# Kernel tuning notes

Hardware: AMD Instinct MI355X
Metric: run time of the kernel (lower is better)

The kernel has to match this reference:

```python
import jax, jax.numpy as jnp
import numpy as np

D_MODEL = 1024
NUM_HEADS = 8
D_K = D_MODEL // NUM_HEADS
NEG_INF = -1e9
EPS = 1e-6


def setup_inputs() -> dict:
    key = jax.random.key(0)
    ks = jax.random.split(key, 10)
    B, S = 4, 2048
    scale = 1.0 / np.sqrt(D_MODEL)
    return {
        "queries": jax.random.normal(ks[0], (B, S, D_MODEL), jnp.float32),
        "keys": jax.random.normal(ks[1], (B, S, D_MODEL), jnp.float32),
        "values": jax.random.normal(ks[2], (B, S, D_MODEL), jnp.float32),
        "Wq": jax.random.normal(ks[3], (D_MODEL, D_MODEL), jnp.float32) * scale,
        "bq": jnp.zeros((D_MODEL,), jnp.float32),
        "Wk": jax.random.normal(ks[4], (D_MODEL, D_MODEL), jnp.float32) * scale,
        "bk": jnp.zeros((D_MODEL,), jnp.float32),
        "Wv": jax.random.normal(ks[5], (D_MODEL, D_MODEL), jnp.float32) * scale,
        "bv": jnp.zeros((D_MODEL,), jnp.float32),
        "gamma": jnp.ones((D_MODEL,), jnp.float32),
        "beta": jnp.zeros((D_MODEL,), jnp.float32),
    }


def _split_heads(x, B, S):
    # [B,S,D] -> [B,H,S,d_k]
    return x.reshape(B, S, NUM_HEADS, D_K).transpose(0, 2, 1, 3)


def reference(queries, keys, values, Wq, bq, Wk, bk, Wv, bv, gamma, beta):
    B, S, _ = queries.shape
    Q = _split_heads(queries @ Wq + bq, B, S)
    K = _split_heads(keys @ Wk + bk, B, keys.shape[1])
    V = _split_heads(values @ Wv + bv, B, values.shape[1])
    scores = jnp.einsum("bhqd,bhkd->bhqk", Q, K) / jnp.sqrt(jnp.float32(D_K))
    # causal mask (lower triangular kept)
    Sk = scores.shape[-1]
    mask = jnp.tril(jnp.ones((scores.shape[-2], Sk), dtype=bool))
    scores = jnp.where(mask, scores, jnp.float32(NEG_INF))
    attn = jax.nn.softmax(scores, axis=-1)
    # dropout disabled (training=False)
    out = jnp.einsum("bhqk,bhkd->bhqd", attn, V)
    out = out.transpose(0, 2, 1, 3).reshape(B, S, D_MODEL)
    resid = out + queries
    mu = jnp.mean(resid, axis=-1, keepdims=True)
    var = jnp.var(resid, axis=-1, keepdims=True)
    normed = (resid - mu) / jnp.sqrt(var + EPS)
    return normed * gamma + beta
```

## Files before the change

### kernel.cpp

```cpp
#include <hip/hip_runtime.h>
#include <hip/hip_bf16.h>
#include <stdint.h>

#define D_MODEL 1024
#define S_LEN   2048
#define BATCH   4
#define NH      8
#define DK      128

typedef __attribute__((ext_vector_type(8))) __bf16 bf16x8;
typedef __attribute__((ext_vector_type(4))) float  f32x4;

__device__ __forceinline__ f32x4 mfma16(bf16x8 a, bf16x8 b, f32x4 c) {
  return __builtin_amdgcn_mfma_f32_16x16x32_bf16(a, b, c, 0, 0, 0);
}

__device__ __forceinline__ void gld_lds16(const void* g, void* l) {
  __builtin_amdgcn_global_load_lds(
      (const __attribute__((address_space(1))) void*)g,
      (__attribute__((address_space(3))) void*)l, 16, 0, 0);
}

#define ATTN_SCALE 0.08838834764831845f

__global__ __launch_bounds__(256) void cvt_kernel(
    const float* __restrict__ x0, const float* __restrict__ x1,
    const float* __restrict__ x2, __hip_bfloat16* __restrict__ out) {
  const size_t N = (size_t)BATCH * S_LEN * D_MODEL;
  const int w = blockIdx.y;
  const float* src = (w == 0) ? x0 : (w == 1) ? x1 : x2;
  __hip_bfloat16* dst = out + (size_t)w * N;
  const size_t i = ((size_t)blockIdx.x * 256 + threadIdx.x) * 4;
  const float4 v = *(const float4*)(src + i);
  *(__hip_bfloat162*)(dst + i)     = __float22bfloat162_rn(make_float2(v.x, v.y));
  *(__hip_bfloat162*)(dst + i + 2) = __float22bfloat162_rn(make_float2(v.z, v.w));
}

__global__ void wtrans_kernel(const float* __restrict__ Wq,
                              const float* __restrict__ Wk,
                              const float* __restrict__ Wv,
                              __hip_bfloat16* __restrict__ Wt) {
  __shared__ __hip_bfloat16 tile[32][33];
  const int w = blockIdx.z;
  const float* src = (w == 0) ? Wq : (w == 1) ? Wk : Wv;
  const float sc = (w == 0) ? ATTN_SCALE : 1.0f;
  __hip_bfloat16* dst = Wt + (size_t)w * D_MODEL * D_MODEL;
  const int tx = threadIdx.x, ty = threadIdx.y;
  int x = blockIdx.x * 32 + tx;
  int y = blockIdx.y * 32 + ty;
  for (int i = 0; i < 32; i += 8)
    tile[ty + i][tx] = __float2bfloat16(src[(size_t)(y + i) * D_MODEL + x] * sc);
  __syncthreads();
  x = blockIdx.y * 32 + tx;
  y = blockIdx.x * 32 + ty;
  for (int i = 0; i < 32; i += 8)
    dst[(size_t)(y + i) * D_MODEL + x] = tile[tx][ty + i];
}

__global__ __launch_bounds__(256) void qkv_gemm_kernel(
    const __hip_bfloat16* __restrict__ Xbf,
    const float* __restrict__ bq, const float* __restrict__ bk,
    const float* __restrict__ bv,
    const __hip_bfloat16* __restrict__ Wt,
    __hip_bfloat16* __restrict__ Qo, __hip_bfloat16* __restrict__ Ko,
    __hip_bfloat16* __restrict__ Vo) {
  const int flat = blockIdx.x;
  const int xcd  = flat & 7;
  const int idx  = flat >> 3;
  const int n_t  = idx & 7;
  const int mg   = idx >> 3;
  const int pair = xcd * 24 + mg;
  const int which = pair >> 6;
  const int m_t   = pair & 63;

  const size_t N = (size_t)BATCH * S_LEN * D_MODEL;
  const __hip_bfloat16* X = Xbf + (size_t)which * N;
  const __hip_bfloat16* W = Wt + (size_t)which * D_MODEL * D_MODEL;
  const float* bias = (which == 0) ? bq : (which == 1) ? bk : bv;
  const float bscale = (which == 0) ? ATTN_SCALE : 1.0f;

  __shared__ __align__(16) char smem[128 * 136 * 2];
  __hip_bfloat16* Asm = (__hip_bfloat16*)smem;
  __hip_bfloat16* Bsm = Asm + 128 * 64;
  __hip_bfloat16* Cb  = (__hip_bfloat16*)smem;

  const int tid  = threadIdx.x;
  const int lane = tid & 63;
  const int wv   = tid >> 6;
  const int lo16 = lane & 15;
  const int hi4  = lane >> 4;
  const int m0 = m_t * 128;
  const int n0 = n_t * 128;
  const int wm = (wv >> 1) * 64;
  const int wn = (wv & 1) * 64;

  f32x4 acc[4][4];
  const f32x4 z4 = {0.f, 0.f, 0.f, 0.f};
  for (int i = 0; i < 4; ++i)
    for (int j = 0; j < 4; ++j) acc[i][j] = z4;

  for (int k0 = 0; k0 < D_MODEL; k0 += 64) {
    __syncthreads();
    for (int it = 0; it < 4; ++it) {
      const int cbase = it * 256 + wv * 64;
      const int c = cbase + lane;
      const int row = c >> 3;
      const int kc = ((c & 7) ^ (row & 7)) * 8;
      gld_lds16(X + (size_t)(m0 + row) * D_MODEL + k0 + kc, &Asm[cbase * 8]);
      gld_lds16(W + (size_t)(n0 + row) * D_MODEL + k0 + kc, &Bsm[cbase * 8]);
    }
    __syncthreads();

    for (int kk = 0; kk < 2; ++kk) {
      bf16x8 af[4], bfr[4];
      const int sl = (kk * 4 + hi4);
      for (int i = 0; i < 4; ++i) {
        const int lm = wm + 16 * i + lo16;
        af[i] = *(const bf16x8*)&Asm[lm * 64 + ((sl ^ (lm & 7)) * 8)];
      }
      for (int j = 0; j < 4; ++j) {
        const int ln = wn + 16 * j + lo16;
        bfr[j] = *(const bf16x8*)&Bsm[ln * 64 + ((sl ^ (ln & 7)) * 8)];
      }
      for (int i = 0; i < 4; ++i)
        for (int j = 0; j < 4; ++j)
          acc[i][j] = mfma16(af[i], bfr[j], acc[i][j]);
    }
  }

  const int b  = m0 >> 11;
  const int s0 = m0 & (S_LEN - 1);
  const int h  = n0 >> 7;
  const size_t bh = (size_t)(b * NH + h);

  __syncthreads();
  for (int j = 0; j < 4; ++j) {
    const int nl = wn + 16 * j + lo16;
    const float bval = bias[n0 + nl] * bscale;
    for (int i = 0; i < 4; ++i) {
      for (int r = 0; r < 4; ++r) {
        const int lm = wm + 16 * i + hi4 * 4 + r;
        const __hip_bfloat16 ob = __float2bfloat16(acc[i][j][r] + bval);
        if (which == 2) {
          const int col = (lm & 96) + 2 * (lm & 15) + ((lm >> 4) & 1);
          Cb[nl * 136 + col] = ob;
        } else {
          Cb[lm * 136 + nl] = ob;
        }
      }
    }
  }
  __syncthreads();

  if (which == 0) {
    __hip_bfloat16* gq = Qo + (bh * S_LEN + s0) * DK;
    for (int r8 = 0; r8 < 8; ++r8) {
      const int C = r8 * 256 + tid;
      const bf16x8 v = *(const bf16x8*)&Cb[(C >> 4) * 136 + (C & 15) * 8];
      *(bf16x8*)&gq[(size_t)C * 8] = v;
    }
  } else if (which == 1) {
    __hip_bfloat16* gk = Ko + (bh * 64 + (s0 >> 5)) * 4096;
    for (int r8 = 0; r8 < 8; ++r8) {
      const int C = r8 * 256 + tid;
      const int su = C >> 9, Cw = C & 511;
      const bf16x8 v =
          *(const bf16x8*)&Cb[(su * 32 + (Cw & 31)) * 136 + (Cw >> 5) * 8];
      *(bf16x8*)&gk[(size_t)su * 4096 + (Cw >> 5) * 256 + (Cw & 31) * 8] = v;
    }
  } else {
    __hip_bfloat16* gv = Vo + (bh * 64 + (s0 >> 5)) * 4096;
    for (int r8 = 0; r8 < 8; ++r8) {
      const int C = r8 * 256 + tid;
      const int su = C >> 9, Cw = C & 511;
      const bf16x8 v =
          *(const bf16x8*)&Cb[(C & 127) * 136 + su * 32 + (Cw >> 7) * 8];
      *(bf16x8*)&gv[(size_t)su * 4096 + (size_t)Cw * 8] = v;
    }
  }
}

__device__ const uint32_t ATTN_TBL[24] = {
  79, 95, 32,
  78, 94, 33,
  77, 93, 34,
  76, 92, 35,
  75, 91, 36,
  39, 72, 88,
  38, 73, 89,
  37, 74, 90
};

__global__ __launch_bounds__(256, 3) void attn_kernel(
    const __hip_bfloat16* __restrict__ Qw, const __hip_bfloat16* __restrict__ Kw,
    const __hip_bfloat16* __restrict__ Vtw, __hip_bfloat16* __restrict__ Og,
    float* __restrict__ partO, float* __restrict__ lsumP) {
  const int bid = blockIdx.x;
  const int q8  = bid & 255;
  const int rr  = bid >> 8;
  const int bh  = q8 & 31;
  const int jrow = q8 >> 5;
  const int h   = bh & 7;
  const int b   = bh >> 3;
  const uint32_t wi = ATTN_TBL[jrow * 3 + rr];
  const int  t     = wi & 15;
  const int  chnk  = (wi >> 4) & 1;
  const bool split = (wi >> 5) == 2;
  const int  half  = 2 * t + 2;
  const int  st0   = (split && chnk == 1) ? half : 0;
  const int  stN   = (split && chnk == 0) ? half : (4 * t + 4);

  const int tid  = threadIdx.x;
  const int lane = tid & 63;
  const int wv   = tid >> 6;
  const int lo16 = lane & 15;
  const int hi4  = lane >> 4;

  const int qrow0 = t * 128 + wv * 32;
  const int ns_w  = 4 * t + wv + 1;

  const size_t bhp = (size_t)(b * NH + h);
  const __hip_bfloat16* Qp = Qw + bhp * S_LEN * DK;
  const __hip_bfloat16* Kp = Kw + bhp * S_LEN * DK;
  const __hip_bfloat16* Vp = Vtw + bhp * S_LEN * DK;

  __shared__ __align__(16) __hip_bfloat16 Ksm[2][32 * 128];
  __shared__ __align__(16) __hip_bfloat16 Psm[4][32 * 40];

  bf16x8 qf[2][4];
  for (int m = 0; m < 2; ++m)
    for (int kk = 0; kk < 4; ++kk)
      qf[m][kk] = *(const bf16x8*)&Qp[(size_t)(qrow0 + m * 16 + lo16) * DK +
                                      kk * 32 + hi4 * 8];

  f32x4 oacc[2][8];
  const f32x4 z4 = {0.f, 0.f, 0.f, 0.f};
  for (int m = 0; m < 2; ++m)
    for (int j = 0; j < 8; ++j) oacc[m][j] = z4;
  float lsum[2][4];
  for (int m = 0; m < 2; ++m)
    for (int i = 0; i < 4; ++i) lsum[m][i] = 0.f;

  const __hip_bfloat16* kbase[2];
#pragma unroll
  for (int it = 0; it < 2; ++it)
    kbase[it] = Kp + (size_t)(it * 256 + tid) * 8;
  auto stage = [&](int st, int buf) {
#pragma unroll
    for (int it = 0; it < 2; ++it) {
      const int cb = (it * 256 + wv * 64) * 8;
      gld_lds16(kbase[it] + ((size_t)st << 12), &Ksm[buf][cb]);
    }
  };

  stage(st0, 0);

  int bsel = 0;
  for (int st = st0; st < stN; ++st) {
    asm volatile("s_waitcnt vmcnt(0)" ::: "memory");
    __builtin_amdgcn_s_barrier();
    asm volatile("" ::: "memory");

    const bool act = st < ns_w;

    bf16x8 vf[8];
    if (act) {
      const __hip_bfloat16* vt = Vp + ((size_t)st << 12);
#pragma unroll
      for (int j = 0; j < 8; ++j)
        vf[j] = *(const bf16x8*)&vt[(hi4 * 128 + j * 16 + lo16) * 8];
    }
    if (st + 1 < stN) stage(st + 1, bsel ^ 1);

    if (act) {
      const __hip_bfloat16* Kb = Ksm[bsel];

      bf16x8 kf[2][4];
      for (int kn = 0; kn < 2; ++kn)
        for (int kk = 0; kk < 4; ++kk)
          kf[kn][kk] = *(const bf16x8*)&Kb[((kk * 4 + hi4) * 32 + kn * 16 + lo16) * 8];
      f32x4 sc[2][2];
      for (int m = 0; m < 2; ++m)
        for (int kn = 0; kn < 2; ++kn) {
          f32x4 s4 = z4;
          for (int kk = 0; kk < 4; ++kk)
            s4 = mfma16(qf[m][kk], kf[kn][kk], s4);
          sc[m][kn] = s4;
        }

      const int kv0 = st << 5;
      const bool do_mask = (st == ns_w - 1);
      for (int m = 0; m < 2; ++m) {
        for (int i = 0; i < 4; ++i) {
          const int qg = qrow0 + m * 16 + hi4 * 4 + i;
          float s0 = sc[m][0][i];
          float s1 = sc[m][1][i];
          if (do_mask) {
            if (kv0 + lo16 > qg)      s0 = -1.0e30f;
            if (kv0 + 16 + lo16 > qg) s1 = -1.0e30f;
          }
          const float p0 = __expf(s0 - 8.f);
          const float p1 = __expf(s1 - 8.f);
          lsum[m][i] += p0 + p1;
          const int prw = m * 16 + hi4 * 4 + i;
          *(__hip_bfloat162*)&Psm[wv][prw * 40 + 2 * lo16] =
              __float22bfloat162_rn(make_float2(p0, p1));
        }
      }
      asm volatile("s_waitcnt lgkmcnt(0)" ::: "memory");

      bf16x8 pf[2];
      for (int m = 0; m < 2; ++m)
        pf[m] = *(const bf16x8*)&Psm[wv][(m * 16 + lo16) * 40 + hi4 * 8];
      for (int j = 0; j < 8; ++j) {
        oacc[0][j] = mfma16(pf[0], vf[j], oacc[0][j]);
        oacc[1][j] = mfma16(pf[1], vf[j], oacc[1][j]);
      }
    }
    bsel ^= 1;
  }

  for (int m = 0; m < 2; ++m) {
    for (int i = 0; i < 4; ++i) {
      float l = lsum[m][i];
      l += __shfl_xor(l, 1);
      l += __shfl_xor(l, 2);
      l += __shfl_xor(l, 4);
      l += __shfl_xor(l, 8);
      const int row = wv * 32 + m * 16 + hi4 * 4 + i;
      if (!split) {
        const float inv = 1.0f / l;
        const int qg = t * 128 + row;
        __hip_bfloat16* orow = Og + ((size_t)b * S_LEN + qg) * D_MODEL + h * DK;
        for (int j = 0; j < 8; ++j)
          orow[j * 16 + lo16] = __float2bfloat16(oacc[m][j][i] * inv);
      } else {
        const int pidx = bh * 8 + (t - 8);
        float* prow = partO +
            (((size_t)chnk * 256 + pidx) * 128 + row) * 128;
        for (int j = 0; j < 8; ++j)
          prow[j * 16 + lo16] = oacc[m][j][i];
        if (lo16 == 0)
          lsumP[(chnk * 256 + pidx) * 128 + row] = l;
      }
    }
  }
}

__global__ __launch_bounds__(256) void ln_kernel(
    const __hip_bfloat16* __restrict__ Og, const float* __restrict__ partO,
    const float* __restrict__ lsumP, const float* __restrict__ resid_in,
    const float* __restrict__ gamma, const float* __restrict__ beta,
    float* __restrict__ out) {
  const int row  = blockIdx.x;
  const int b    = row >> 11;
  const int srow = row & (S_LEN - 1);
  const int tile = srow >> 7;
  const int tid  = threadIdx.x;
  const int base = tid * 4;
  const float4 q4 = *(const float4*)(resid_in + (size_t)row * D_MODEL + base);
  float v[4];
  if (tile < 8) {
    const __hip_bfloat16* orow = Og + (size_t)row * D_MODEL;
    const ushort4 o4 = *(const ushort4*)(orow + base);
    v[0] = __bfloat162float(*(const __hip_bfloat16*)&o4.x) + q4.x;
    v[1] = __bfloat162float(*(const __hip_bfloat16*)&o4.y) + q4.y;
    v[2] = __bfloat162float(*(const __hip_bfloat16*)&o4.z) + q4.z;
    v[3] = __bfloat162float(*(const __hip_bfloat16*)&o4.w) + q4.w;
  } else {
    const int h    = base >> 7;
    const int rin  = srow & 127;
    const int pidx = (b * 8 + h) * 8 + (tile - 8);
    const size_t off = ((size_t)pidx * 128 + rin) * 128 + (base & 127);
    const float4 p0 = *(const float4*)(partO + off);
    const float4 p1 = *(const float4*)(partO + (size_t)256 * 128 * 128 + off);
    const float l = lsumP[pidx * 128 + rin] +
                    lsumP[256 * 128 + pidx * 128 + rin];
    const float inv = 1.0f / l;
    v[0] = (p0.x + p1.x) * inv + q4.x;
    v[1] = (p0.y + p1.y) * inv + q4.y;
    v[2] = (p0.z + p1.z) * inv + q4.z;
    v[3] = (p0.w + p1.w) * inv + q4.w;
  }
  float s = v[0] + v[1] + v[2] + v[3];
  float ss = v[0] * v[0] + v[1] * v[1] + v[2] * v[2] + v[3] * v[3];
  for (int m = 1; m < 64; m <<= 1) { s += __shfl_xor(s, m); ss += __shfl_xor(ss, m); }
  __shared__ float red[8];
  const int wv = tid >> 6, lane = tid & 63;
  if (lane == 0) { red[wv] = s; red[4 + wv] = ss; }
  __syncthreads();
  s  = red[0] + red[1] + red[2] + red[3];
  ss = red[4] + red[5] + red[6] + red[7];
  const float mu  = s * (1.0f / D_MODEL);
  const float var = ss * (1.0f / D_MODEL) - mu * mu;
  const float rstd = rsqrtf(var + 1e-6f);
  const float4 g4 = *(const float4*)(gamma + base);
  const float4 b4 = *(const float4*)(beta + base);
  float4 o;
  o.x = (v[0] - mu) * rstd * g4.x + b4.x;
  o.y = (v[1] - mu) * rstd * g4.y + b4.y;
  o.z = (v[2] - mu) * rstd * g4.z + b4.z;
  o.w = (v[3] - mu) * rstd * g4.w + b4.w;
  *(float4*)(out + (size_t)row * D_MODEL + base) = o;
}

extern "C" void kernel_launch(void* const* d_in, const int* in_sizes, int n_in,
                              void* d_out, int out_size, void* d_ws, size_t ws_size,
                              hipStream_t stream) {
  const float* queries = (const float*)d_in[0];
  const float* keys    = (const float*)d_in[1];
  const float* values  = (const float*)d_in[2];
  const float* Wq = (const float*)d_in[3];
  const float* bq = (const float*)d_in[4];
  const float* Wk = (const float*)d_in[5];
  const float* bk = (const float*)d_in[6];
  const float* Wv = (const float*)d_in[7];
  const float* bv = (const float*)d_in[8];
  const float* gamma = (const float*)d_in[9];
  const float* beta  = (const float*)d_in[10];

  char* ws = (char*)d_ws;
  const size_t N = (size_t)BATCH * S_LEN * D_MODEL;
  const size_t WT_BYTES  = (size_t)3 * D_MODEL * D_MODEL * 2;
  const size_t XBF_BYTES = (size_t)3 * N * 2;
  const size_t QKV_BYTES = (size_t)BATCH * NH * S_LEN * DK * 2;
  const size_t OG_BYTES  = (size_t)BATCH * S_LEN * D_MODEL * 2;
  __hip_bfloat16* Wt  = (__hip_bfloat16*)ws;
  __hip_bfloat16* Xbf = (__hip_bfloat16*)(ws + WT_BYTES);
  __hip_bfloat16* Ogs = (__hip_bfloat16*)(ws + WT_BYTES);
  float* partO = (float*)(ws + WT_BYTES + OG_BYTES);
  float* lsumP = (float*)ws;
  __hip_bfloat16* Qws = (__hip_bfloat16*)(ws + WT_BYTES + XBF_BYTES);
  __hip_bfloat16* Kws = (__hip_bfloat16*)(ws + WT_BYTES + XBF_BYTES + QKV_BYTES);
  __hip_bfloat16* Vws = (__hip_bfloat16*)(ws + WT_BYTES + XBF_BYTES + 2 * QKV_BYTES);

  cvt_kernel<<<dim3((unsigned)(N / 1024), 3), 256, 0, stream>>>(queries, keys, values, Xbf);
  wtrans_kernel<<<dim3(32, 32, 3), dim3(32, 8), 0, stream>>>(Wq, Wk, Wv, Wt);
  qkv_gemm_kernel<<<dim3(1536), 256, 0, stream>>>(
      Xbf, bq, bk, bv, Wt, Qws, Kws, Vws);
  attn_kernel<<<dim3(768), 256, 0, stream>>>(Qws, Kws, Vws, Ogs, partO, lsumP);
  ln_kernel<<<dim3(BATCH * S_LEN), 256, 0, stream>>>(Ogs, partO, lsumP, queries,
                                                     gamma, beta, (float*)d_out);
}
```

Measured before the change: 314.4 us.

## Double-buffer QKV GEMM LDS staging and merge conversion kernels into one launch

The QKV projection GEMM now uses two LDS buffers, issuing the async global-to-LDS loads for the next K tile before computing on the current one. This is meant to overlap memory latency with MFMA work, and it needs one barrier per iteration instead of two. The input-cast and weight-transpose kernels are also merged into a single prep launch to save one kernel launch and fill the GPU better. The cost is double the LDS per block (64KB), which can lower occupancy. The single barrier also relies on vmcnt(0) plus s_barrier to keep reads and writes of the two buffers from racing.

Result: no change. 315.1 us (+0.2%).

```diff
diff --git a/kernel.cpp b/kernel.cpp
--- a/kernel.cpp
+++ b/kernel.cpp
@@ -23,38 +23,39 @@
 
 #define ATTN_SCALE 0.08838834764831845f
 
-__global__ __launch_bounds__(256) void cvt_kernel(
-    const float* __restrict__ x0, const float* __restrict__ x1,
-    const float* __restrict__ x2, __hip_bfloat16* __restrict__ out) {
-  const size_t N = (size_t)BATCH * S_LEN * D_MODEL;
-  const int w = blockIdx.y;
-  const float* src = (w == 0) ? x0 : (w == 1) ? x1 : x2;
-  __hip_bfloat16* dst = out + (size_t)w * N;
-  const size_t i = ((size_t)blockIdx.x * 256 + threadIdx.x) * 4;
-  const float4 v = *(const float4*)(src + i);
-  *(__hip_bfloat162*)(dst + i)     = __float22bfloat162_rn(make_float2(v.x, v.y));
-  *(__hip_bfloat162*)(dst + i + 2) = __float22bfloat162_rn(make_float2(v.z, v.w));
-}
-
-__global__ void wtrans_kernel(const float* __restrict__ Wq,
-                              const float* __restrict__ Wk,
-                              const float* __restrict__ Wv,
-                              __hip_bfloat16* __restrict__ Wt) {
+__global__ __launch_bounds__(256) void prep_kernel(
+    const float* __restrict__ q, const float* __restrict__ k,
+    const float* __restrict__ v, const float* __restrict__ Wq,
+    const float* __restrict__ Wk, const float* __restrict__ Wv,
+    __hip_bfloat16* __restrict__ Xbf, __hip_bfloat16* __restrict__ Wt) {
   __shared__ __hip_bfloat16 tile[32][33];
-  const int w = blockIdx.z;
-  const float* src = (w == 0) ? Wq : (w == 1) ? Wk : Wv;
-  const float sc = (w == 0) ? ATTN_SCALE : 1.0f;
-  __hip_bfloat16* dst = Wt + (size_t)w * D_MODEL * D_MODEL;
-  const int tx = threadIdx.x, ty = threadIdx.y;
-  int x = blockIdx.x * 32 + tx;
-  int y = blockIdx.y * 32 + ty;
-  for (int i = 0; i < 32; i += 8)
-    tile[ty + i][tx] = __float2bfloat16(src[(size_t)(y + i) * D_MODEL + x] * sc);
-  __syncthreads();
-  x = blockIdx.y * 32 + tx;
-  y = blockIdx.x * 32 + ty;
-  for (int i = 0; i < 32; i += 8)
-    dst[(size_t)(y + i) * D_MODEL + x] = tile[tx][ty + i];
+  const int w  = blockIdx.y;
+  const int tid = threadIdx.x;
+  if (blockIdx.x < 8192) {
+    const size_t N = (size_t)BATCH * S_LEN * D_MODEL;
+    const float* src = (w == 0) ? q : (w == 1) ? k : v;
+    __hip_bfloat16* dst = Xbf + (size_t)w * N;
+    const size_t i = ((size_t)blockIdx.x * 256 + tid) * 4;
+    const float4 vv = *(const float4*)(src + i);
+    *(__hip_bfloat162*)(dst + i)     = __float22bfloat162_rn(make_float2(vv.x, vv.y));
+    *(__hip_bfloat162*)(dst + i + 2) = __float22bfloat162_rn(make_float2(vv.z, vv.w));
+  } else {
+    const int bidx = blockIdx.x - 8192;
+    const int bx = bidx & 31, by = bidx >> 5;
+    const float* src = (w == 0) ? Wq : (w == 1) ? Wk : Wv;
+    const float sc = (w == 0) ? ATTN_SCALE : 1.0f;
+    __hip_bfloat16* dst = Wt + (size_t)w * D_MODEL * D_MODEL;
+    const int tx = tid & 31, ty = tid >> 5;
+    int x = bx * 32 + tx;
+    int y = by * 32 + ty;
+    for (int i = 0; i < 32; i += 8)
+      tile[ty + i][tx] = __float2bfloat16(src[(size_t)(y + i) * D_MODEL + x] * sc);
+    __syncthreads();
+    x = by * 32 + tx;
+    y = bx * 32 + ty;
+    for (int i = 0; i < 32; i += 8)
+      dst[(size_t)(y + i) * D_MODEL + x] = tile[tx][ty + i];
+  }
 }
 
 __global__ __launch_bounds__(256) void qkv_gemm_kernel(
@@ -79,10 +80,8 @@
   const float* bias = (which == 0) ? bq : (which == 1) ? bk : bv;
   const float bscale = (which == 0) ? ATTN_SCALE : 1.0f;
 
-  __shared__ __align__(16) char smem[128 * 136 * 2];
-  __hip_bfloat16* Asm = (__hip_bfloat16*)smem;
-  __hip_bfloat16* Bsm = Asm + 128 * 64;
-  __hip_bfloat16* Cb  = (__hip_bfloat16*)smem;
+  __shared__ __align__(16) __hip_bfloat16 SMEM[4][128 * 64];
+  __hip_bfloat16* Cb = (__hip_bfloat16*)SMEM;
 
   const int tid  = threadIdx.x;
   const int lane = tid & 63;
@@ -99,18 +98,30 @@
   for (int i = 0; i < 4; ++i)
     for (int j = 0; j < 4; ++j) acc[i][j] = z4;
 
-  for (int k0 = 0; k0 < D_MODEL; k0 += 64) {
-    __syncthreads();
+  auto stage = [&](int t, int buf) {
+#pragma unroll
     for (int it = 0; it < 4; ++it) {
       const int cbase = it * 256 + wv * 64;
       const int c = cbase + lane;
       const int row = c >> 3;
       const int kc = ((c & 7) ^ (row & 7)) * 8;
-      gld_lds16(X + (size_t)(m0 + row) * D_MODEL + k0 + kc, &Asm[cbase * 8]);
-      gld_lds16(W + (size_t)(n0 + row) * D_MODEL + k0 + kc, &Bsm[cbase * 8]);
-    }
-    __syncthreads();
-
+      gld_lds16(X + (size_t)(m0 + row) * D_MODEL + t * 64 + kc,
+                &SMEM[2 * buf][cbase * 8]);
+      gld_lds16(W + (size_t)(n0 + row) * D_MODEL + t * 64 + kc,
+                &SMEM[2 * buf + 1][cbase * 8]);
+    }
+  };
+
+  stage(0, 0);
+  int bsel = 0;
+  for (int t = 0; t < 16; ++t) {
+    asm volatile("s_waitcnt vmcnt(0)" ::: "memory");
+    __builtin_amdgcn_s_barrier();
+    asm volatile("" ::: "memory");
+    if (t + 1 < 16) stage(t + 1, bsel ^ 1);
+
+    const __hip_bfloat16* Asm = SMEM[2 * bsel];
+    const __hip_bfloat16* Bsm = SMEM[2 * bsel + 1];
     for (int kk = 0; kk < 2; ++kk) {
       bf16x8 af[4], bfr[4];
       const int sl = (kk * 4 + hi4);
@@ -126,6 +137,7 @@
         for (int j = 0; j < 4; ++j)
           acc[i][j] = mfma16(af[i], bfr[j], acc[i][j]);
     }
+    bsel ^= 1;
   }
 
   const int b  = m0 >> 11;
@@ -434,8 +446,8 @@
   __hip_bfloat16* Kws = (__hip_bfloat16*)(ws + WT_BYTES + XBF_BYTES + QKV_BYTES);
   __hip_bfloat16* Vws = (__hip_bfloat16*)(ws + WT_BYTES + XBF_BYTES + 2 * QKV_BYTES);
 
-  cvt_kernel<<<dim3((unsigned)(N / 1024), 3), 256, 0, stream>>>(queries, keys, values, Xbf);
-  wtrans_kernel<<<dim3(32, 32, 3), dim3(32, 8), 0, stream>>>(Wq, Wk, Wv, Wt);
+  prep_kernel<<<dim3(8192 + 1024, 3), 256, 0, stream>>>(
+      queries, keys, values, Wq, Wk, Wv, Xbf, Wt);
   qkv_gemm_kernel<<<dim3(1536), 256, 0, stream>>>(
       Xbf, bq, bk, bv, Wt, Qws, Kws, Vws);
   attn_kernel<<<dim3(768), 256, 0, stream>>>(Qws, Kws, Vws, Ogs, partO, lsumP);
```
